# Optimization experiments

Hardware: AMD Instinct MI355X
Metric: run time of the kernel (lower is better)

The kernel has to match this reference:

```python
import jax, jax.numpy as jnp
import numpy as np

B, N, NCTX, DIM, H, DH, NMEM = 2, 1024, 2048, 1024, 16, 64, 16


def setup_inputs() -> dict:
    key = jax.random.key(0)
    ks = jax.random.split(key, 24)
    r = lambda i, shape, s=1.0: jax.random.normal(ks[i], shape, dtype=jnp.float32) * s
    w = 0.02  # linear weight scale
    return {
        "x": r(0, (B, N, DIM)),
        "context": r(1, (2, B, NCTX, DIM)),
        "wq1": r(2, (DIM, H * DH), w), "wk1": r(3, (DIM, H * DH), w), "wv1": r(4, (DIM, H * DH), w),
        "wq2": r(5, (DIM, H * DH), w), "wk2": r(6, (DIM, H * DH), w), "wv2": r(7, (DIM, H * DH), w),
        "th_pre1": r(8, (H, H), 0.25), "th_post1": r(9, (H, H), 0.25),
        "th_pre2": r(10, (H, H), 0.25), "th_post2": r(11, (H, H), 0.25),
        "scale1": jnp.full((1, H, 1, 1), -3.0, jnp.float32) + r(12, (1, H, 1, 1), 0.05),
        "scale2": jnp.full((1, H, 1, 1), -3.0, jnp.float32) + r(13, (1, H, 1, 1), 0.05),
        "mem_k1": r(14, (H, NMEM, DH)), "mem_v1": r(15, (H, NMEM, DH)),
        "mem_k2": r(16, (H, NMEM, DH)), "mem_v2": r(17, (H, NMEM, DH)),
        "hs1": jnp.ones((1, H, 1, 1), jnp.float32) + r(18, (1, H, 1, 1), 0.05),
        "hs2": jnp.ones((1, H, 1, 1), jnp.float32) + r(19, (1, H, 1, 1), 0.05),
        "wo1": r(20, (H * DH, DIM), w), "wo2": r(21, (H * DH, DIM), w),
    }


def _l2norm(t):
    # F.normalize: t / max(||t||, eps)
    n = jnp.linalg.norm(t, axis=-1, keepdims=True)
    return t / jnp.maximum(n, 1e-12)


def _split_heads(t, b):
    # [b, n, h*d] -> [b, h, n, d]
    return t.reshape(b, -1, H, DH).transpose(0, 2, 1, 3)


def _attend(x, kv, wq, wk, wv, th_pre, th_post, scale_p, mem_k, mem_v, hs, wo):
    b, n, _ = x.shape
    q = _split_heads(x @ wq, b)    # [b,h,n,d]
    k = _split_heads(kv @ wk, b)   # [b,h,j,d]
    v = _split_heads(kv @ wv, b)
    # memory key/values prepended
    k = jnp.concatenate([jnp.broadcast_to(mem_k[None], (b, H, NMEM, DH)), k], axis=2)
    v = jnp.concatenate([jnp.broadcast_to(mem_v[None], (b, H, NMEM, DH)), v], axis=2)
    # qk-norm with learned per-head temperature: scale = 1 / clamp(exp(p), min=0.01)
    q, k = _l2norm(q), _l2norm(k)
    scale = 1.0 / jnp.maximum(jnp.exp(scale_p), 0.01)
    dots = jnp.einsum('bhid,bhjd->bhij', q, k) * scale
    # talking heads: 1x1 Conv2d over head channel == head-mixing matmul
    dots = jnp.einsum('gh,bhij->bgij', th_pre, dots)
    attn = jax.nn.softmax(dots, axis=-1)
    attn = jnp.einsum('gh,bhij->bgij', th_post, attn)
    out = jnp.einsum('bhij,bhjd->bhid', attn, v) * hs  # head_scale
    out = out.transpose(0, 2, 1, 3).reshape(b, n, H * DH)
    return out @ wo


def reference(x, context, wq1, wk1, wv1, wq2, wk2, wv2,
              th_pre1, th_post1, th_pre2, th_post2,
              scale1, scale2, mem_k1, mem_v1, mem_k2, mem_v2,
              hs1, hs2, wo1, wo2):
    o1 = _attend(x, context[0], wq1, wk1, wv1, th_pre1, th_post1, scale1, mem_k1, mem_v1, hs1, wo1)
    o2 = _attend(x, context[1], wq2, wk2, wv2, th_pre2, th_post2, scale2, mem_k2, mem_v2, hs2, wo2)
    return o1 + o2
```

## Files before the change

kernel.cpp:

```cpp
#include <hip/hip_runtime.h>
#include <hip/hip_bf16.h>

#define Bb    2
#define Nn    1024
#define NCTXc 2048
#define DIMd  1024
#define Hh    16
#define DHd   64
#define NMEM  16
#define Jv    (NMEM + NCTXc)
#define JP    2112
#define HJP   (Hh * JP)
#define L2E   1.44269504088896f
#define LDH   1048

typedef _Float16 f16;
typedef _Float16 half8 __attribute__((ext_vector_type(8)));
typedef _Float16 half4 __attribute__((ext_vector_type(4)));
typedef float    f32x4 __attribute__((ext_vector_type(4)));

__device__ __forceinline__ float bf2f(unsigned short u){
  union { unsigned int i; float f; } v; v.i = ((unsigned)u) << 16; return v.f;
}
__device__ __forceinline__ float fin(float v){
  v = (v == v) ? v : 0.f;
  return fminf(fmaxf(v, -65504.f), 65504.f);
}
__device__ __forceinline__ float ldin(const void* p, long i, int isf32){
  return isf32 ? ((const float*)p)[i] : bf2f(((const unsigned short*)p)[i]);
}
__device__ __forceinline__ half8 h8zero(){
  half8 v;
  #pragma unroll
  for (int j = 0; j < 8; j++) v[j] = (f16)0.f;
  return v;
}
__device__ __forceinline__ void gload16(const f16* g, f16* l){
  __builtin_amdgcn_global_load_lds(
      (const __attribute__((address_space(1))) unsigned int*)g,
      (__attribute__((address_space(3))) unsigned int*)l, 16, 0, 0);
}

__global__ void detect_dtype(const void* __restrict__ p, int* __restrict__ flag, int n){
  const unsigned short* ub = (const unsigned short*)p;
  const float* fp = (const float*)p;
  int t = threadIdx.x;
  float bb = 0.f, bf = 0.f;
  for (int i = t; i < n; i += 64){
    float vb = bf2f(ub[i]);
    if (!(vb == vb) || fabsf(vb) > 1000.f) bb += 1.f;
    float vf = fp[i];
    if (!(vf == vf) || fabsf(vf) > 1000.f) bf += 1.f;
  }
  #pragma unroll
  for (int off = 32; off; off >>= 1){ bb += __shfl_xor(bb, off); bf += __shfl_xor(bf, off); }
  if (t == 0) *flag = (bf < bb) ? 1 : 0;
}

__global__ __launch_bounds__(256) void cvt_any(const void* __restrict__ in, f16* __restrict__ out,
                                               long n, long off, const int* __restrict__ flag){
  int isf = *flag;
  long stride = (long)gridDim.x * 256;
  for (long i = (long)blockIdx.x * 256 + threadIdx.x; i < n; i += stride)
    out[i] = (f16)fin(ldin(in, off + i, isf));
}

__global__ __launch_bounds__(256) void cvt32_any(const void* __restrict__ in, float* __restrict__ out,
                                                 long n, const int* __restrict__ flag){
  int isf = *flag;
  long stride = (long)gridDim.x * 256;
  for (long i = (long)blockIdx.x * 256 + threadIdx.x; i < n; i += stride)
    out[i] = fin(ldin(in, i, isf));
}

__global__ __launch_bounds__(256) void transpose_any(const void* __restrict__ in,
                                                     f16* __restrict__ out,
                                                     int Cc, long ldo,
                                                     const int* __restrict__ flag){
  __shared__ f16 tile[32][33];
  int isf = *flag;
  int r0 = blockIdx.y * 32, c0 = blockIdx.x * 32;
  int tr = threadIdx.x >> 5, tc = threadIdx.x & 31;
  #pragma unroll
  for (int k = 0; k < 4; k++){
    int r = tr + k * 8;
    tile[r][tc] = (f16)fin(ldin(in, (long)(r0 + r) * Cc + c0 + tc, isf));
  }
  __syncthreads();
  #pragma unroll
  for (int k = 0; k < 4; k++){
    int r = tr + k * 8;
    out[(long)(c0 + r) * ldo + r0 + tc] = tile[tc][r];
  }
}

__global__ __launch_bounds__(256) void gemm128(
    const f16* __restrict__ A, const f16* __restrict__ Bt, f16* __restrict__ C,
    int K, long lda, long ldb, long ldc)
{
  __shared__ __align__(16) f16 As[128 * 32];
  __shared__ __align__(16) f16 Bs[128 * 32];
  long m0 = (long)blockIdx.y * 128, n0 = (long)blockIdx.x * 128;
  int t = threadIdx.x;
  int wave = t >> 6, lane = t & 63;
  int wm = (wave >> 1) * 64, wn = (wave & 1) * 64;
  int fr = lane & 15, fq = lane >> 4;
  int sr = t >> 2, scc = (t & 3) * 8;

  f32x4 acc[4][4];
  #pragma unroll
  for (int a = 0; a < 4; a++)
    #pragma unroll
    for (int b = 0; b < 4; b++) acc[a][b] = (f32x4){0.f, 0.f, 0.f, 0.f};

  const f16* Ap  = A  + (m0 + sr) * lda + scc;
  const f16* Ap2 = Ap + 64 * lda;
  const f16* Bp  = Bt + (n0 + sr) * ldb + scc;
  const f16* Bp2 = Bp + 64 * ldb;
  f16* Ad  = As + t * 8;
  f16* Ad2 = As + 2048 + t * 8;
  f16* Bd  = Bs + t * 8;
  f16* Bd2 = Bs + 2048 + t * 8;

  for (int k0 = 0; k0 < K; k0 += 32){
    __syncthreads();
    gload16(Ap  + k0, Ad);
    gload16(Ap2 + k0, Ad2);
    gload16(Bp  + k0, Bd);
    gload16(Bp2 + k0, Bd2);
    __syncthreads();
    half8 bfr[4];
    #pragma unroll
    for (int tj = 0; tj < 4; tj++)
      bfr[tj] = *(const half8*)&Bs[(wn + 16 * tj + fr) * 32 + fq * 8];
    #pragma unroll
    for (int ti = 0; ti < 4; ti++){
      half8 af = *(const half8*)&As[(wm + 16 * ti + fr) * 32 + fq * 8];
      #pragma unroll
      for (int tj = 0; tj < 4; tj++)
        acc[ti][tj] = __builtin_amdgcn_mfma_f32_16x16x32_f16(af, bfr[tj], acc[ti][tj], 0, 0, 0);
    }
  }
  #pragma unroll
  for (int ti = 0; ti < 4; ti++)
    #pragma unroll
    for (int tj = 0; tj < 4; tj++)
      #pragma unroll
      for (int r = 0; r < 4; r++){
        long row = m0 + wm + 16 * ti + fq * 4 + r;
        long col = n0 + wn + 16 * tj + fr;
        C[row * ldc + col] = (f16)acc[ti][tj][r];
      }
}

__global__ __launch_bounds__(256) void gemm128_dyn(
    const f16* __restrict__ A, const f16* __restrict__ Bt, void* __restrict__ C,
    int K, long lda, long ldb, long ldc, const int* __restrict__ flag)
{
  int isf = *flag;
  __shared__ __align__(16) f16 As[128 * 32];
  __shared__ __align__(16) f16 Bs[128 * 32];
  long m0 = (long)blockIdx.y * 128, n0 = (long)blockIdx.x * 128;
  int t = threadIdx.x;
  int wave = t >> 6, lane = t & 63;
  int wm = (wave >> 1) * 64, wn = (wave & 1) * 64;
  int fr = lane & 15, fq = lane >> 4;
  int sr = t >> 2, scc = (t & 3) * 8;

  f32x4 acc[4][4];
  #pragma unroll
  for (int a = 0; a < 4; a++)
    #pragma unroll
    for (int b = 0; b < 4; b++) acc[a][b] = (f32x4){0.f, 0.f, 0.f, 0.f};

  const f16* Ap  = A  + (m0 + sr) * lda + scc;
  const f16* Ap2 = Ap + 64 * lda;
  const f16* Bp  = Bt + (n0 + sr) * ldb + scc;
  const f16* Bp2 = Bp + 64 * ldb;
  f16* Ad  = As + t * 8;
  f16* Ad2 = As + 2048 + t * 8;
  f16* Bd  = Bs + t * 8;
  f16* Bd2 = Bs + 2048 + t * 8;

  for (int k0 = 0; k0 < K; k0 += 32){
    __syncthreads();
    gload16(Ap  + k0, Ad);
    gload16(Ap2 + k0, Ad2);
    gload16(Bp  + k0, Bd);
    gload16(Bp2 + k0, Bd2);
    __syncthreads();
    half8 bfr[4];
    #pragma unroll
    for (int tj = 0; tj < 4; tj++)
      bfr[tj] = *(const half8*)&Bs[(wn + 16 * tj + fr) * 32 + fq * 8];
    #pragma unroll
    for (int ti = 0; ti < 4; ti++){
      half8 af = *(const half8*)&As[(wm + 16 * ti + fr) * 32 + fq * 8];
      #pragma unroll
      for (int tj = 0; tj < 4; tj++)
        acc[ti][tj] = __builtin_amdgcn_mfma_f32_16x16x32_f16(af, bfr[tj], acc[ti][tj], 0, 0, 0);
    }
  }
  #pragma unroll
  for (int ti = 0; ti < 4; ti++)
    #pragma unroll
    for (int tj = 0; tj < 4; tj++)
      #pragma unroll
      for (int r = 0; r < 4; r++){
        long row = m0 + wm + 16 * ti + fq * 4 + r;
        long col = n0 + wn + 16 * tj + fr;
        float v = acc[ti][tj][r];
        if (isf) ((float*)C)[row * ldc + col] = v;
        else     ((__hip_bfloat16*)C)[row * ldc + col] = __float2bfloat16(v);
      }
}

__global__ __launch_bounds__(256) void gemm_bt(
    const f16* __restrict__ A, const f16* __restrict__ Bt, f16* __restrict__ C,
    int K, long lda, long ldb, long ldc,
    long sAb, long sBb, long sCb, long sAh, long sBh, long sCh, int nh)
{
  int z = blockIdx.z;
  int zb = z / nh, zh = z - zb * nh;
  A  += (long)zb * sAb + (long)zh * sAh;
  Bt += (long)zb * sBb + (long)zh * sBh;
  C  += (long)zb * sCb + (long)zh * sCh;
  long m0 = (long)blockIdx.y * 64, n0 = (long)blockIdx.x * 64;

  __shared__ f16 As[64][40];
  __shared__ f16 Bs[64][40];
  __shared__ __align__(16) f16 Cs[64 * 64];
  int t = threadIdx.x;
  int wave = t >> 6, lane = t & 63;
  int wm = (wave >> 1) * 32, wn = (wave & 1) * 32;
  int fr = lane & 15, fq = lane >> 4;
  int srow = t >> 2, scol = (t & 3) * 8;

  f32x4 acc[2][2];
  #pragma unroll
  for (int a = 0; a < 2; a++)
    #pragma unroll
    for (int b = 0; b < 2; b++) acc[a][b] = (f32x4){0.f, 0.f, 0.f, 0.f};

  for (int k0 = 0; k0 < K; k0 += 32){
    half8 avv = *(const half8*)(A  + (m0 + srow) * lda + k0 + scol);
    half8 bvv = *(const half8*)(Bt + (n0 + srow) * ldb + k0 + scol);
    __syncthreads();
    *(half8*)&As[srow][scol] = avv;
    *(half8*)&Bs[srow][scol] = bvv;
    __syncthreads();
    #pragma unroll
    for (int ti = 0; ti < 2; ti++){
      half8 af = *(const half8*)&As[wm + 16 * ti + fr][fq * 8];
      #pragma unroll
      for (int tj = 0; tj < 2; tj++){
        half8 bf = *(const half8*)&Bs[wn + 16 * tj + fr][fq * 8];
        acc[ti][tj] = __builtin_amdgcn_mfma_f32_16x16x32_f16(af, bf, acc[ti][tj], 0, 0, 0);
      }
    }
  }
  #pragma unroll
  for (int ti = 0; ti < 2; ti++)
    #pragma unroll
    for (int tj = 0; tj < 2; tj++)
      #pragma unroll
      for (int r = 0; r < 4; r++)
        Cs[(wm + 16 * ti + fq * 4 + r) * 64 + wn + 16 * tj + fr] = (f16)acc[ti][tj][r];
  __syncthreads();
  #pragma unroll
  for (int it = 0; it < 2; it++){
    int idx = t + it * 256;
    int row = idx >> 3, c8 = (idx & 7) * 8;
    *(half8*)(C + (m0 + row) * ldc + n0 + c8) = *(const half8*)&Cs[row * 64 + c8];
  }
}

__global__ __launch_bounds__(256) void qn_build(const f16* __restrict__ qp, f16* __restrict__ qn,
                                                const float* __restrict__ scale_p){
  int row = blockIdx.x;
  int wave = threadIdx.x >> 6, lane = threadIdx.x & 63;
  #pragma unroll
  for (int hh = 0; hh < 4; hh++){
    int h = wave * 4 + hh;
    float v = (float)qp[(long)row * 2048 + h * 64 + lane];
    float ss = v * v;
    #pragma unroll
    for (int off = 32; off; off >>= 1) ss += __shfl_xor(ss, off);
    float sc = 1.0f / fmaxf(__expf(scale_p[h]), 0.01f);
    float o = v / fmaxf(sqrtf(ss), 1e-12f) * sc;
    qn[(long)row * 1024 + h * 64 + lane] = (f16)o;
  }
}

__global__ __launch_bounds__(256) void kbuf_build(const f16* __restrict__ kp,
                                                  const f16* __restrict__ mem_k,
                                                  f16* __restrict__ kbuf){
  int id = blockIdx.x * 4 + (threadIdx.x >> 6);
  int lane = threadIdx.x & 63;
  int h = id & 15; int bj = id >> 4; int j = bj % JP; int b = bj / JP;
  float v;
  if (j < NMEM)              v = (float)mem_k[(h * NMEM + j) * 64 + lane];
  else if (j < NMEM + NCTXc) v = (float)kp[((long)b * NCTXc + (j - NMEM)) * 2048 + h * 64 + lane];
  else                       v = 0.f;
  float ss = v * v;
  #pragma unroll
  for (int off = 32; off; off >>= 1) ss += __shfl_xor(ss, off);
  float o = v / fmaxf(sqrtf(ss), 1e-12f);
  kbuf[((long)b * JP + j) * 1024 + h * 64 + lane] = (f16)o;
}

__global__ __launch_bounds__(256) void vt_build(const f16* __restrict__ vp,
                                                const f16* __restrict__ mem_v,
                                                f16* __restrict__ vt){
  __shared__ f16 tile[64][72];
  int id = blockIdx.x;
  int jt = id % (JP / 64); int h = (id / (JP / 64)) & 15; int b = id / (16 * (JP / 64));
  int j0 = jt * 64;
  int t = threadIdx.x;
  #pragma unroll
  for (int rep = 0; rep < 2; rep++){
    int idx = t + rep * 256;
    int jj = idx >> 3, c8 = (idx & 7) * 8;
    int j = j0 + jj;
    half8 v;
    if (j < NMEM){
      v = *(const half8*)(mem_v + (h * NMEM + j) * 64 + c8);
    } else if (j < NMEM + NCTXc){
      v = *(const half8*)(vp + ((long)b * NCTXc + (j - NMEM)) * 2048 + h * 64 + c8);
    } else {
      v = h8zero();
    }
    *(half8*)&tile[jj][c8] = v;
  }
  __syncthreads();
  #pragma unroll
  for (int rep = 0; rep < 2; rep++){
    int idx = t + rep * 256;
    int d = idx >> 3, j8 = (idx & 7) * 8;
    half8 o;
    #pragma unroll
    for (int k = 0; k < 8; k++) o[k] = tile[j8 + k][d];
    *(half8*)(vt + (((long)(b * 16 + h) * 64 + d) * JP) + j0 + j8) = o;
  }
}

__global__ __launch_bounds__(512) void softmax_mfma(
    f16* __restrict__ S,
    const float* __restrict__ th_pre,
    const float* __restrict__ th_post,
    const float* __restrict__ hs)
{
  __shared__ f16 tile[16 * LDH];
  __shared__ float msh[8][16], lsh[8][16];
  __shared__ float Mf[16], Li[16];

  int t = threadIdx.x, wave = t >> 6, lane = t & 63;
  int r16 = lane & 15;
  int hb4 = (lane >> 4) * 4;
  int sr  = t >> 5, sc = t & 31;
  f16* Srow = S + (long)blockIdx.x * HJP;

  half4 ahi, alo;
  #pragma unroll
  for (int j = 0; j < 4; j++){
    float a = th_pre[r16 * 16 + hb4 + j];
    ahi[j] = (f16)a; alo[j] = (f16)(a - (float)ahi[j]);
  }

  float m[4], l[4];
  #pragma unroll
  for (int r = 0; r < 4; r++){ m[r] = -1e30f; l[r] = 0.f; }

  half4 msave[17];
  const f32x4 z4 = (f32x4){0.f, 0.f, 0.f, 0.f};

  #pragma unroll
  for (int it = 0; it < 5; it++){
    int c8 = sc + it * 32;
    if (c8 < 130)
      *(half8*)&tile[sr * LDH + c8 * 8] = *(const half8*)(Srow + (long)sr * JP + c8 * 8);
  }
  __syncthreads();
  #pragma unroll
  for (int cc = 0; cc < 9; cc++){
    int c = wave + cc * 8;
    if (c < 65){
      int lc = c * 16 + r16;
      half4 b;
      #pragma unroll
      for (int j = 0; j < 4; j++) b[j] = tile[(hb4 + j) * LDH + lc];
      f32x4 acc = __builtin_amdgcn_mfma_f32_16x16x16f16(alo, b, z4, 0, 0, 0);
      acc = __builtin_amdgcn_mfma_f32_16x16x16f16(ahi, b, acc, 0, 0, 0);
      half4 hh;
      #pragma unroll
      for (int r = 0; r < 4; r++){
        float u = fminf(fmaxf(acc[r], -60.f), 78.f);
        m[r] = fmaxf(m[r], u);
        l[r] += exp2f(u * L2E);
        hh[r] = (f16)u;
      }
      msave[cc] = hh;
    }
  }
  __syncthreads();
  #pragma unroll
  for (int it = 0; it < 4; it++){
    int c8 = sc + it * 32;
    *(half8*)&tile[sr * LDH + c8 * 8] = *(const half8*)(Srow + (long)sr * JP + 1040 + c8 * 8);
  }
  __syncthreads();
  #pragma unroll
  for (int cc = 0; cc < 8; cc++){
    int c = 65 + wave + cc * 8;
    int lc = c * 16 - 1040 + r16;
    half4 b;
    #pragma unroll
    for (int j = 0; j < 4; j++) b[j] = tile[(hb4 + j) * LDH + lc];
    f32x4 acc = __builtin_amdgcn_mfma_f32_16x16x16f16(alo, b, z4, 0, 0, 0);
    acc = __builtin_amdgcn_mfma_f32_16x16x16f16(ahi, b, acc, 0, 0, 0);
    half4 hh;
    #pragma unroll
    for (int r = 0; r < 4; r++){
      float u = fminf(fmaxf(acc[r], -60.f), 78.f);
      m[r] = fmaxf(m[r], u);
      l[r] += exp2f(u * L2E);
      hh[r] = (f16)u;
    }
    msave[9 + cc] = hh;
  }

  #pragma unroll
  for (int off = 1; off < 16; off <<= 1){
    #pragma unroll
    for (int r = 0; r < 4; r++){
      m[r] = fmaxf(m[r], __shfl_xor(m[r], off));
      l[r] += __shfl_xor(l[r], off);
    }
  }
  if (r16 == 0){
    #pragma unroll
    for (int r = 0; r < 4; r++){ msh[wave][hb4 + r] = m[r]; lsh[wave][hb4 + r] = l[r]; }
  }
  __syncthreads();
  if (t < 16){
    float mf_ = msh[0][t], lf = lsh[0][t];
    #pragma unroll
    for (int w = 1; w < 8; w++){ mf_ = fmaxf(mf_, msh[w][t]); lf += lsh[w][t]; }
    Mf[t] = mf_;
    Li[t] = fin(exp2f(mf_ * L2E) / lf);
  }
  __syncthreads();

  half4 chi, clo;
  float hsv = hs[r16];
  #pragma unroll
  for (int j = 0; j < 4; j++){
    float cc2 = th_post[r16 * 16 + hb4 + j] * hsv * Li[hb4 + j];
    chi[j] = (f16)cc2; clo[j] = (f16)(cc2 - (float)chi[j]);
  }
  float mf[4];
  #pragma unroll
  for (int r = 0; r < 4; r++) mf[r] = Mf[hb4 + r];

  #pragma unroll
  for (int cc = 0; cc < 9; cc++){
    int c = wave + cc * 8;
    if (c < 65){
      half4 h4 = msave[cc];
      half4 ehi, elo;
      #pragma unroll
      for (int r = 0; r < 4; r++){
        float e = exp2f(((float)h4[r] - mf[r]) * L2E);
        ehi[r] = (f16)e; elo[r] = (f16)(e - (float)ehi[r]);
      }
      f32x4 o = __builtin_amdgcn_mfma_f32_16x16x16f16(chi, ehi, z4, 0, 0, 0);
      o = __builtin_amdgcn_mfma_f32_16x16x16f16(clo, ehi, o, 0, 0, 0);
      o = __builtin_amdgcn_mfma_f32_16x16x16f16(chi, elo, o, 0, 0, 0);
      int col = c * 16 + r16;
      #pragma unroll
      for (int r = 0; r < 4; r++) Srow[(hb4 + r) * JP + col] = (f16)o[r];
    }
  }
  #pragma unroll
  for (int cc = 0; cc < 8; cc++){
    int c = 65 + wave + cc * 8;
    half4 h4 = msave[9 + cc];
    half4 ehi, elo;
    #pragma unroll
    for (int r = 0; r < 4; r++){
      float e = exp2f(((float)h4[r] - mf[r]) * L2E);
      ehi[r] = (f16)e; elo[r] = (f16)(e - (float)ehi[r]);
    }
    f32x4 o = __builtin_amdgcn_mfma_f32_16x16x16f16(chi, ehi, z4, 0, 0, 0);
    o = __builtin_amdgcn_mfma_f32_16x16x16f16(clo, ehi, o, 0, 0, 0);
    o = __builtin_amdgcn_mfma_f32_16x16x16f16(chi, elo, o, 0, 0, 0);
    int col = c * 16 + r16;
    #pragma unroll
    for (int r = 0; r < 4; r++) Srow[(hb4 + r) * JP + col] = (f16)o[r];
  }
}

extern "C" void kernel_launch(void* const* d_in, const int* in_sizes, int n_in,
                              void* d_out, int out_size, void* d_ws, size_t ws_size,
                              hipStream_t stream)
{
  (void)in_sizes; (void)n_in; (void)out_size; (void)ws_size;
  int* flag = (int*)d_ws;
  f16* ws   = (f16*)d_ws + 8;
  f16* wT   = ws;
  f16* woT  = wT   + 6291456;
  f16* qn   = woT  + 2097152;
  f16* kbuf = qn   + 4194304;
  f16* vt   = kbuf + 4325376;
  f16* av   = vt   + 4325376;
  f16* memc = av   + 4194304;
  float* parc = (float*)(memc + 65536);
  f16* S    = (f16*)(parc + 1088);
  f16* tmpkv = S;
  f16* tmpq  = S + 8388608;
  f16* xf    = S + 12582912;
  f16* cxf   = S + 14680064;

  detect_dtype<<<1, 64, 0, stream>>>(d_in[0], flag, 4096);

  for (int i = 0; i < 4; i++)
    cvt_any<<<16, 256, 0, stream>>>(d_in[14 + i], memc + (long)i * 16384, 16384, 0, flag);
  {
    const int  src[8] = {8, 9, 10, 11, 12, 13, 18, 19};
    const long off[8] = {0, 256, 512, 768, 1024, 1040, 1056, 1072};
    const long cnt[8] = {256, 256, 256, 256, 16, 16, 16, 16};
    for (int i = 0; i < 8; i++)
      cvt32_any<<<1, 256, 0, stream>>>(d_in[src[i]], parc + off[i], cnt[i], flag);
  }

  {
    const int slot[6] = {0, 2, 3, 1, 4, 5};
    for (int i = 0; i < 6; i++)
      transpose_any<<<dim3(32, 32), 256, 0, stream>>>(d_in[2 + i],
                                                      wT + (long)slot[i] * 1048576, 1024, 1024, flag);
  }
  for (int L = 0; L < 2; L++)
    transpose_any<<<dim3(32, 32), 256, 0, stream>>>(d_in[20 + L],
                                                    woT + (long)L * 1024, 1024, 2048, flag);

  cvt_any<<<1024, 256, 0, stream>>>(d_in[0], xf, 2097152, 0, flag);
  gemm128<<<dim3(16, 16), 256, 0, stream>>>(xf, wT, tmpq, 1024, 1024, 1024, 2048);
  for (int L = 0; L < 2; L++)
    qn_build<<<Bb * Nn, 256, 0, stream>>>(tmpq + (long)L * 1024, qn + (long)L * 2097152,
                                          parc + 1024 + (long)L * 16);

  for (int L = 0; L < 2; L++){
    const float* thpre  = parc + (long)L * 512;
    const float* thpost = parc + (long)L * 512 + 256;
    const float* hsp    = parc + 1056 + (long)L * 16;
    const f16* mem_k = memc + (long)(2 * L) * 16384;
    const f16* mem_v = memc + (long)(2 * L + 1) * 16384;
    const long ctxOff = (long)L * Bb * NCTXc * DIMd;
    const f16* qnL = qn + (long)L * 2097152;

    cvt_any<<<2048, 256, 0, stream>>>(d_in[1], cxf, 4194304, ctxOff, flag);
    gemm128<<<dim3(16, 32), 256, 0, stream>>>(cxf, wT + (long)(2 + 2 * L) * 1048576,
                                              tmpkv, 1024, 1024, 1024, 2048);
    kbuf_build<<<Bb * JP * Hh / 4, 256, 0, stream>>>(tmpkv, mem_k, kbuf);
    vt_build<<<Bb * Hh * (JP / 64), 256, 0, stream>>>(tmpkv + 1024, mem_v, vt);

    gemm_bt<<<dim3(JP / 64, Nn / 64, Bb * Hh), 256, 0, stream>>>(qnL, kbuf, S, 64,
        1024, 1024, HJP,
        (long)Nn * 1024, (long)JP * 1024, (long)Nn * HJP,
        64, 64, JP, Hh);

    softmax_mfma<<<Bb * Nn, 512, 0, stream>>>(S, thpre, thpost, hsp);

    gemm_bt<<<dim3(1, Nn / 64, Bb * Hh), 256, 0, stream>>>(S, vt,
        av + (long)L * 1024, JP,
        HJP, JP, 2048,
        (long)Nn * HJP, (long)Hh * 64 * JP, (long)Nn * 2048,
        JP, (long)64 * JP, 64, Hh);
  }

  gemm128_dyn<<<dim3(8, 16), 256, 0, stream>>>(av, woT, d_out, 2048,
      2048, 2048, 1024, flag);
}
```

Baseline: 811.9 us.

## Write QK scores head-interleaved so softmax reads them directly without LDS staging

Replaces the generic batched QK^T GEMM with a dedicated kernel that computes all 16 heads for a 64x16 tile and stores scores interleaved as [row][j][head]. The softmax kernel then loads each half4 of heads straight from global memory instead of staging two half-row tiles through shared memory with extra barriers. It writes normalized probabilities back in the original [head][j] layout and zeroes the padded tail columns explicitly. The risk is that the new score kernel is small per block (16 columns, K=64 per head) and may use MFMA and LDS less efficiently than the old GEMM.

```diff
diff --git a/kernel.cpp b/kernel.cpp
--- a/kernel.cpp
+++ b/kernel.cpp
@@ -12,7 +12,6 @@
 #define JP    2112
 #define HJP   (Hh * JP)
 #define L2E   1.44269504088896f
-#define LDH   1048
 
 typedef _Float16 f16;
 typedef _Float16 half8 __attribute__((ext_vector_type(8)));
@@ -275,6 +274,166 @@
   }
 }
 
+__global__ __launch_bounds__(256) void score_h16(
+    const f16* __restrict__ qn, const f16* __restrict__ kbuf, f16* __restrict__ S)
+{
+  __shared__ f16 Aw[4][64 * 72];
+  __shared__ f16 Bw[4][16 * 72];
+  __shared__ __align__(16) f16 Cs[64 * 256];
+  int t = threadIdx.x, wave = t >> 6, lane = t & 63;
+  int fr = lane & 15, fq = lane >> 4;
+  long j0 = (long)blockIdx.x * 16;
+  long i0 = (long)blockIdx.y * 64;
+  int b = blockIdx.z;
+  const f16* qb = qn + ((long)b * Nn + i0) * 1024;
+  const f16* kb = kbuf + ((long)b * JP + j0) * 1024;
+  f16* A = Aw[wave];
+  f16* B = Bw[wave];
+
+  #pragma unroll
+  for (int hh = 0; hh < 4; hh++){
+    int h = wave * 4 + hh;
+    #pragma unroll
+    for (int it = 0; it < 8; it++){
+      int idx = lane + it * 64;
+      int row = idx >> 3, c8 = (idx & 7) * 8;
+      *(half8*)&A[row * 72 + c8] = *(const half8*)(qb + (long)row * 1024 + h * 64 + c8);
+    }
+    #pragma unroll
+    for (int it = 0; it < 2; it++){
+      int idx = lane + it * 64;
+      int row = idx >> 3, c8 = (idx & 7) * 8;
+      *(half8*)&B[row * 72 + c8] = *(const half8*)(kb + (long)row * 1024 + h * 64 + c8);
+    }
+    #pragma unroll
+    for (int ti = 0; ti < 4; ti++){
+      f32x4 acc = (f32x4){0.f, 0.f, 0.f, 0.f};
+      #pragma unroll
+      for (int k0 = 0; k0 < 64; k0 += 32){
+        half8 af = *(const half8*)&A[(ti * 16 + fr) * 72 + k0 + fq * 8];
+        half8 bf = *(const half8*)&B[fr * 72 + k0 + fq * 8];
+        acc = __builtin_amdgcn_mfma_f32_16x16x32_f16(af, bf, acc, 0, 0, 0);
+      }
+      #pragma unroll
+      for (int r = 0; r < 4; r++)
+        Cs[(ti * 16 + fq * 4 + r) * 256 + fr * 16 + h] = (f16)acc[r];
+    }
+  }
+  __syncthreads();
+  #pragma unroll
+  for (int it = 0; it < 8; it++){
+    int f = it * 256 + t;
+    int row = f >> 5, w8 = (f & 31) * 8;
+    *(half8*)(S + (((long)b * Nn + i0 + row) * JP + j0) * 16 + w8) = *(const half8*)&Cs[row * 256 + w8];
+  }
+}
+
+__global__ __launch_bounds__(512) void softmax_mfma(
+    f16* __restrict__ S,
+    const float* __restrict__ th_pre,
+    const float* __restrict__ th_post,
+    const float* __restrict__ hs)
+{
+  __shared__ float msh[8][16], lsh[8][16];
+  __shared__ float Mf[16], Li[16];
+
+  int t = threadIdx.x, wave = t >> 6, lane = t & 63;
+  int r16 = lane & 15;
+  int hb4 = (lane >> 4) * 4;
+  f16* Srow = S + (long)blockIdx.x * HJP;
+
+  half4 ahi, alo;
+  #pragma unroll
+  for (int j = 0; j < 4; j++){
+    float a = th_pre[r16 * 16 + hb4 + j];
+    ahi[j] = (f16)a; alo[j] = (f16)(a - (float)ahi[j]);
+  }
+
+  float m[4], l[4];
+  #pragma unroll
+  for (int r = 0; r < 4; r++){ m[r] = -1e30f; l[r] = 0.f; }
+
+  half4 msave[17];
+  const f32x4 z4 = (f32x4){0.f, 0.f, 0.f, 0.f};
+
+  #pragma unroll
+  for (int cc = 0; cc < 17; cc++){
+    int c = wave + cc * 8;
+    if (c < 129){
+      int lc = c * 16 + r16;
+      half4 b = *(const half4*)(Srow + (long)lc * 16 + hb4);
+      f32x4 acc = __builtin_amdgcn_mfma_f32_16x16x16f16(alo, b, z4, 0, 0, 0);
+      acc = __builtin_amdgcn_mfma_f32_16x16x16f16(ahi, b, acc, 0, 0, 0);
+      half4 hh;
+      #pragma unroll
+      for (int r = 0; r < 4; r++){
+        float u = fminf(fmaxf(acc[r], -60.f), 78.f);
+        m[r] = fmaxf(m[r], u);
+        l[r] += exp2f(u * L2E);
+        hh[r] = (f16)u;
+      }
+      msave[cc] = hh;
+    }
+  }
+
+  #pragma unroll
+  for (int off = 1; off < 16; off <<= 1){
+    #pragma unroll
+    for (int r = 0; r < 4; r++){
+      m[r] = fmaxf(m[r], __shfl_xor(m[r], off));
+      l[r] += __shfl_xor(l[r], off);
+    }
+  }
+  if (r16 == 0){
+    #pragma unroll
+    for (int r = 0; r < 4; r++){ msh[wave][hb4 + r] = m[r]; lsh[wave][hb4 + r] = l[r]; }
+  }
+  __syncthreads();
+  if (t < 16){
+    float mf_ = msh[0][t], lf = lsh[0][t];
+    #pragma unroll
+    for (int w = 1; w < 8; w++){ mf_ = fmaxf(mf_, msh[w][t]); lf += lsh[w][t]; }
+    Mf[t] = mf_;
+    Li[t] = fin(exp2f(mf_ * L2E) / lf);
+  }
+  __syncthreads();
+
+  half4 chi, clo;
+  float hsv = hs[r16];
+  #pragma unroll
+  for (int j = 0; j < 4; j++){
+    float cc2 = th_post[r16 * 16 + hb4 + j] * hsv * Li[hb4 + j];
+    chi[j] = (f16)cc2; clo[j] = (f16)(cc2 - (float)chi[j]);
+  }
+  float mf[4];
+  #pragma unroll
+  for (int r = 0; r < 4; r++) mf[r] = Mf[hb4 + r];
+
+  for (int idx = t; idx < 16 * 48; idx += 512){
+    int g = idx / 48, col = 2064 + idx - g * 48;
+    Srow[g * JP + col] = (f16)0.f;
+  }
+  #pragma unroll
+  for (int cc = 0; cc < 17; cc++){
+    int c = wave + cc * 8;
+    if (c < 129){
+      half4 h4 = msave[cc];
+      half4 ehi, elo;
+      #pragma unroll
+      for (int r = 0; r < 4; r++){
+        float e = exp2f(((float)h4[r] - mf[r]) * L2E);
+        ehi[r] = (f16)e; elo[r] = (f16)(e - (float)ehi[r]);
+      }
+      f32x4 o = __builtin_amdgcn_mfma_f32_16x16x16f16(chi, ehi, z4, 0, 0, 0);
+      o = __builtin_amdgcn_mfma_f32_16x16x16f16(clo, ehi, o, 0, 0, 0);
+      o = __builtin_amdgcn_mfma_f32_16x16x16f16(chi, elo, o, 0, 0, 0);
+      int col = c * 16 + r16;
+      #pragma unroll
+      for (int r = 0; r < 4; r++) Srow[(hb4 + r) * JP + col] = (f16)o[r];
+    }
+  }
+}
+
 __global__ __launch_bounds__(256) void qn_build(const f16* __restrict__ qp, f16* __restrict__ qn,
                                                 const float* __restrict__ scale_p){
   int row = blockIdx.x;
@@ -341,162 +500,6 @@
     #pragma unroll
     for (int k = 0; k < 8; k++) o[k] = tile[j8 + k][d];
     *(half8*)(vt + (((long)(b * 16 + h) * 64 + d) * JP) + j0 + j8) = o;
-  }
-}
-
-__global__ __launch_bounds__(512) void softmax_mfma(
-    f16* __restrict__ S,
-    const float* __restrict__ th_pre,
-    const float* __restrict__ th_post,
-    const float* __restrict__ hs)
-{
-  __shared__ f16 tile[16 * LDH];
-  __shared__ float msh[8][16], lsh[8][16];
-  __shared__ float Mf[16], Li[16];
-
-  int t = threadIdx.x, wave = t >> 6, lane = t & 63;
-  int r16 = lane & 15;
-  int hb4 = (lane >> 4) * 4;
-  int sr  = t >> 5, sc = t & 31;
-  f16* Srow = S + (long)blockIdx.x * HJP;
-
-  half4 ahi, alo;
-  #pragma unroll
-  for (int j = 0; j < 4; j++){
-    float a = th_pre[r16 * 16 + hb4 + j];
-    ahi[j] = (f16)a; alo[j] = (f16)(a - (float)ahi[j]);
-  }
-
-  float m[4], l[4];
-  #pragma unroll
-  for (int r = 0; r < 4; r++){ m[r] = -1e30f; l[r] = 0.f; }
-
-  half4 msave[17];
-  const f32x4 z4 = (f32x4){0.f, 0.f, 0.f, 0.f};
-
-  #pragma unroll
-  for (int it = 0; it < 5; it++){
-    int c8 = sc + it * 32;
-    if (c8 < 130)
-      *(half8*)&tile[sr * LDH + c8 * 8] = *(const half8*)(Srow + (long)sr * JP + c8 * 8);
-  }
-  __syncthreads();
-  #pragma unroll
-  for (int cc = 0; cc < 9; cc++){
-    int c = wave + cc * 8;
-    if (c < 65){
-      int lc = c * 16 + r16;
-      half4 b;
-      #pragma unroll
-      for (int j = 0; j < 4; j++) b[j] = tile[(hb4 + j) * LDH + lc];
-      f32x4 acc = __builtin_amdgcn_mfma_f32_16x16x16f16(alo, b, z4, 0, 0, 0);
-      acc = __builtin_amdgcn_mfma_f32_16x16x16f16(ahi, b, acc, 0, 0, 0);
-      half4 hh;
-      #pragma unroll
-      for (int r = 0; r < 4; r++){
-        float u = fminf(fmaxf(acc[r], -60.f), 78.f);
-        m[r] = fmaxf(m[r], u);
-        l[r] += exp2f(u * L2E);
-        hh[r] = (f16)u;
-      }
-      msave[cc] = hh;
-    }
-  }
-  __syncthreads();
-  #pragma unroll
-  for (int it = 0; it < 4; it++){
-    int c8 = sc + it * 32;
-    *(half8*)&tile[sr * LDH + c8 * 8] = *(const half8*)(Srow + (long)sr * JP + 1040 + c8 * 8);
-  }
-  __syncthreads();
-  #pragma unroll
-  for (int cc = 0; cc < 8; cc++){
-    int c = 65 + wave + cc * 8;
-    int lc = c * 16 - 1040 + r16;
-    half4 b;
-    #pragma unroll
-    for (int j = 0; j < 4; j++) b[j] = tile[(hb4 + j) * LDH + lc];
-    f32x4 acc = __builtin_amdgcn_mfma_f32_16x16x16f16(alo, b, z4, 0, 0, 0);
-    acc = __builtin_amdgcn_mfma_f32_16x16x16f16(ahi, b, acc, 0, 0, 0);
-    half4 hh;
-    #pragma unroll
-    for (int r = 0; r < 4; r++){
-      float u = fminf(fmaxf(acc[r], -60.f), 78.f);
-      m[r] = fmaxf(m[r], u);
-      l[r] += exp2f(u * L2E);
-      hh[r] = (f16)u;
-    }
-    msave[9 + cc] = hh;
-  }
-
-  #pragma unroll
-  for (int off = 1; off < 16; off <<= 1){
-    #pragma unroll
-    for (int r = 0; r < 4; r++){
-      m[r] = fmaxf(m[r], __shfl_xor(m[r], off));
-      l[r] += __shfl_xor(l[r], off);
-    }
-  }
-  if (r16 == 0){
-    #pragma unroll
-    for (int r = 0; r < 4; r++){ msh[wave][hb4 + r] = m[r]; lsh[wave][hb4 + r] = l[r]; }
-  }
-  __syncthreads();
-  if (t < 16){
-    float mf_ = msh[0][t], lf = lsh[0][t];
-    #pragma unroll
-    for (int w = 1; w < 8; w++){ mf_ = fmaxf(mf_, msh[w][t]); lf += lsh[w][t]; }
-    Mf[t] = mf_;
-    Li[t] = fin(exp2f(mf_ * L2E) / lf);
-  }
-  __syncthreads();
-
-  half4 chi, clo;
-  float hsv = hs[r16];
-  #pragma unroll
-  for (int j = 0; j < 4; j++){
-    float cc2 = th_post[r16 * 16 + hb4 + j] * hsv * Li[hb4 + j];
-    chi[j] = (f16)cc2; clo[j] = (f16)(cc2 - (float)chi[j]);
-  }
-  float mf[4];
-  #pragma unroll
-  for (int r = 0; r < 4; r++) mf[r] = Mf[hb4 + r];
-
-  #pragma unroll
-  for (int cc = 0; cc < 9; cc++){
-    int c = wave + cc * 8;
-    if (c < 65){
-      half4 h4 = msave[cc];
-      half4 ehi, elo;
-      #pragma unroll
-      for (int r = 0; r < 4; r++){
-        float e = exp2f(((float)h4[r] - mf[r]) * L2E);
-        ehi[r] = (f16)e; elo[r] = (f16)(e - (float)ehi[r]);
-      }
-      f32x4 o = __builtin_amdgcn_mfma_f32_16x16x16f16(chi, ehi, z4, 0, 0, 0);
-      o = __builtin_amdgcn_mfma_f32_16x16x16f16(clo, ehi, o, 0, 0, 0);
-      o = __builtin_amdgcn_mfma_f32_16x16x16f16(chi, elo, o, 0, 0, 0);
-      int col = c * 16 + r16;
-      #pragma unroll
-      for (int r = 0; r < 4; r++) Srow[(hb4 + r) * JP + col] = (f16)o[r];
-    }
-  }
-  #pragma unroll
-  for (int cc = 0; cc < 8; cc++){
-    int c = 65 + wave + cc * 8;
-    half4 h4 = msave[9 + cc];
-    half4 ehi, elo;
-    #pragma unroll
-    for (int r = 0; r < 4; r++){
-      float e = exp2f(((float)h4[r] - mf[r]) * L2E);
-      ehi[r] = (f16)e; elo[r] = (f16)(e - (float)ehi[r]);
-    }
-    f32x4 o = __builtin_amdgcn_mfma_f32_16x16x16f16(chi, ehi, z4, 0, 0, 0);
-    o = __builtin_amdgcn_mfma_f32_16x16x16f16(clo, ehi, o, 0, 0, 0);
-    o = __builtin_amdgcn_mfma_f32_16x16x16f16(chi, elo, o, 0, 0, 0);
-    int col = c * 16 + r16;
-    #pragma unroll
-    for (int r = 0; r < 4; r++) Srow[(hb4 + r) * JP + col] = (f16)o[r];
   }
 }
 
@@ -564,10 +567,7 @@
     kbuf_build<<<Bb * JP * Hh / 4, 256, 0, stream>>>(tmpkv, mem_k, kbuf);
     vt_build<<<Bb * Hh * (JP / 64), 256, 0, stream>>>(tmpkv + 1024, mem_v, vt);
 
-    gemm_bt<<<dim3(JP / 64, Nn / 64, Bb * Hh), 256, 0, stream>>>(qnL, kbuf, S, 64,
-        1024, 1024, HJP,
-        (long)Nn * 1024, (long)JP * 1024, (long)Nn * HJP,
-        64, 64, JP, Hh);
+    score_h16<<<dim3(129, Nn / 64, Bb), 256, 0, stream>>>(qnL, kbuf, S);
 
     softmax_mfma<<<Bb * Nn, 512, 0, stream>>>(S, thpre, thpost, hsp);
 
```

Result: slower. 834.6 us (+2.8%).
